# Optimization experiments

Measured on AMD Instinct MI355X. Metric: run time of the kernel, lower is better.

## Reference

```python
import jax, jax.numpy as jnp
import numpy as np

B, H, S, D = 4, 8, 2048, 64  # batch, heads, seq, head_dim (feature_dim == num_features == D)


def setup_inputs() -> dict:
    key = jax.random.key(0)
    kq, kk, kv, kw = jax.random.split(key, 4)
    return {
        "q": jax.random.normal(kq, (B, H, S, D), dtype=jnp.float32),
        "k": jax.random.normal(kk, (B, H, S, D), dtype=jnp.float32),
        "v": jax.random.normal(kv, (B, H, S, D), dtype=jnp.float32),
        "random_weights": jax.random.normal(kw, (D, D), dtype=jnp.float32),  # [feature_dim, num_features]
    }


def reference(q, k, v, random_weights):
    # F.linear(x, W) == x @ W.T ; W: [feature_dim, num_features]
    qf = jax.nn.relu(jnp.einsum('bnhd,fd->bnhf', q, random_weights))
    kf = jax.nn.relu(jnp.einsum('bnad,fd->bnaf', k, random_weights))
    # full [B, N, S_q, S_kv] score matrix (as the original materializes it)
    scores = jnp.einsum('bnhd,bnad->bnha', qf, kf)
    attn_weights = jax.nn.softmax(scores, axis=-1)
    # NOTE: faithful to the original (buggy) einsum: m is contracted only in attn,
    # so attn_output[b,n,h,d] = v[b,n,h,d] * sum_m attn[b,n,h,m]
    attn_output = jnp.einsum('bnhm,bnhd->bnhd', attn_weights, v)
    return (attn_output, attn_weights)
```

## Files before the change

### kernel.cpp

```cpp
#include <hip/hip_runtime.h>
#include <cstddef>
#include <cstdint>

#define SEQ   2048
#define DIM   64
#define NHEAD 32
#define BM    128
#define BN    128
#define NT    (SEQ / BN)
#define WLD   68

typedef __attribute__((ext_vector_type(8))) short short8v;

__device__ __forceinline__ unsigned short f2bf(float x) {
    union { float f; unsigned u; } v; v.f = x;
    unsigned r = v.u + 0x7FFFu + ((v.u >> 16) & 1u);
    return (unsigned short)(r >> 16);
}
__device__ __forceinline__ float bf2f(unsigned short h) {
    union { unsigned u; float f; } v; v.u = ((unsigned)h) << 16;
    return v.f;
}

__global__ __launch_bounds__(256) void kfsplit_kernel(const float* __restrict__ kin,
                                                      const float* __restrict__ W,
                                                      unsigned short* __restrict__ khg,
                                                      unsigned short* __restrict__ klg)
{
    __shared__ __align__(16) float Ws[64 * WLD];
    const int tid  = threadIdx.x;
    const int head = blockIdx.x >> 4;
    const int r0   = (blockIdx.x & 15) * BM;

    {
        const int f = tid >> 2, cc = (tid & 3) * 16;
        const float* gw = W + f * DIM + cc;
        #pragma unroll
        for (int kk = 0; kk < 4; ++kk)
            *reinterpret_cast<float4*>(&Ws[f * WLD + cc + kk * 4]) =
                *reinterpret_cast<const float4*>(gw + kk * 4);
    }
    __syncthreads();

    const int lane = tid & 63;
    const int wid  = tid >> 6;
    const float* kb = kin + ((size_t)head * SEQ + r0) * DIM;

    float acc0[16], acc1[16];
    #pragma unroll
    for (int j = 0; j < 16; ++j) { acc0[j] = 0.f; acc1[j] = 0.f; }

    for (int d4 = 0; d4 < 16; ++d4) {
        const float4 x0 = *reinterpret_cast<const float4*>(kb + (size_t)lane * DIM + d4 * 4);
        const float4 x1 = *reinterpret_cast<const float4*>(kb + (size_t)(64 + lane) * DIM + d4 * 4);
        #pragma unroll
        for (int j = 0; j < 16; ++j) {
            const float4 w4 = *reinterpret_cast<const float4*>(&Ws[(wid * 16 + j) * WLD + d4 * 4]);
            acc0[j] = fmaf(x0.x, w4.x, fmaf(x0.y, w4.y, fmaf(x0.z, w4.z, fmaf(x0.w, w4.w, acc0[j]))));
            acc1[j] = fmaf(x1.x, w4.x, fmaf(x1.y, w4.y, fmaf(x1.z, w4.z, fmaf(x1.w, w4.w, acc1[j]))));
        }
    }

#define SPLIT_ROW(ACC, ROWOFF)                                                          \
    do {                                                                                \
        unsigned hp[8], lp[8];                                                          \
        _Pragma("unroll")                                                               \
        for (int j2 = 0; j2 < 8; ++j2) {                                                \
            const float kf0 = fmaxf(ACC[2 * j2], 0.f);                                  \
            const float kf1 = fmaxf(ACC[2 * j2 + 1], 0.f);                              \
            const unsigned short h0 = f2bf(kf0), h1 = f2bf(kf1);                        \
            const unsigned short l0 = f2bf(kf0 - bf2f(h0));                             \
            const unsigned short l1 = f2bf(kf1 - bf2f(h1));                             \
            hp[j2] = (unsigned)h0 | ((unsigned)h1 << 16);                               \
            lp[j2] = (unsigned)l0 | ((unsigned)l1 << 16);                               \
        }                                                                               \
        unsigned short* dh = khg + ((size_t)head * SEQ + r0 + (ROWOFF)) * DIM + wid * 16; \
        unsigned short* dl = klg + ((size_t)head * SEQ + r0 + (ROWOFF)) * DIM + wid * 16; \
        uint4 a, b;                                                                     \
        a.x = hp[0]; a.y = hp[1]; a.z = hp[2]; a.w = hp[3];                             \
        b.x = hp[4]; b.y = hp[5]; b.z = hp[6]; b.w = hp[7];                             \
        *reinterpret_cast<uint4*>(dh) = a; *reinterpret_cast<uint4*>(dh + 8) = b;       \
        a.x = lp[0]; a.y = lp[1]; a.z = lp[2]; a.w = lp[3];                             \
        b.x = lp[4]; b.y = lp[5]; b.z = lp[6]; b.w = lp[7];                             \
        *reinterpret_cast<uint4*>(dl) = a; *reinterpret_cast<uint4*>(dl + 8) = b;       \
    } while (0)

    SPLIT_ROW(acc0, lane);
    SPLIT_ROW(acc1, 64 + lane);
#undef SPLIT_ROW
}

__global__ __launch_bounds__(256, 2) void attn_kernel(const float* __restrict__ q,
                                                      const float* __restrict__ W,
                                                      const unsigned short* __restrict__ khg,
                                                      const unsigned short* __restrict__ klg,
                                                      float* __restrict__ out)
{
    __shared__ __align__(16) float lds[13056];
    float* Ws = lds;
    float* qf = lds + 4352;
    unsigned short* khs = reinterpret_cast<unsigned short*>(lds);
    unsigned short* kls = reinterpret_cast<unsigned short*>(lds + 4096);
    float* mbuf = lds + 8192;
    float* lbuf = lds + 8448;

    const int tid  = threadIdx.x;
    const int head = blockIdx.x >> 4;
    const int r0   = (blockIdx.x & 15) * BM;
    const int lane = tid & 63;
    const int wid  = tid >> 6;

    {
        const int f = tid >> 2, cc = (tid & 3) * 16;
        const float* gw = W + f * DIM + cc;
        #pragma unroll
        for (int kk = 0; kk < 4; ++kk)
            *reinterpret_cast<float4*>(&Ws[f * WLD + cc + kk * 4]) =
                *reinterpret_cast<const float4*>(gw + kk * 4);
    }
    __syncthreads();

    {
        const float* qb = q + ((size_t)head * SEQ + r0) * DIM;
        float a0[16], a1[16];
        #pragma unroll
        for (int j = 0; j < 16; ++j) { a0[j] = 0.f; a1[j] = 0.f; }
        for (int d4 = 0; d4 < 16; ++d4) {
            const float4 x0 = *reinterpret_cast<const float4*>(qb + (size_t)lane * DIM + d4 * 4);
            const float4 x1 = *reinterpret_cast<const float4*>(qb + (size_t)(64 + lane) * DIM + d4 * 4);
            #pragma unroll
            for (int j = 0; j < 16; ++j) {
                const float4 w4 = *reinterpret_cast<const float4*>(&Ws[(wid * 16 + j) * WLD + d4 * 4]);
                a0[j] = fmaf(x0.x, w4.x, fmaf(x0.y, w4.y, fmaf(x0.z, w4.z, fmaf(x0.w, w4.w, a0[j]))));
                a1[j] = fmaf(x1.x, w4.x, fmaf(x1.y, w4.y, fmaf(x1.z, w4.z, fmaf(x1.w, w4.w, a1[j]))));
            }
        }
        #pragma unroll
        for (int j = 0; j < 16; ++j) {
            qf[(size_t)lane * WLD + wid * 16 + j]        = fmaxf(a0[j], 0.f);
            qf[(size_t)(64 + lane) * WLD + wid * 16 + j] = fmaxf(a1[j], 0.f);
        }
    }
    __syncthreads();

    const int lr = lane & 15, lh = lane >> 4;
    const int wrow = (wid >> 1) * 64, wcol = (wid & 1) * 64;
    short8v qh[4][2], ql[4][2];
    #pragma unroll
    for (int rf = 0; rf < 4; ++rf)
        #pragma unroll
        for (int ks = 0; ks < 2; ++ks) {
            const float* src = &qf[(size_t)(wrow + rf * 16 + lr) * WLD + ks * 32 + lh * 8];
            short8v h, l;
            #pragma unroll
            for (int e = 0; e < 8; ++e) {
                const float x = src[e];
                const unsigned short hh = f2bf(x);
                h[e] = (short)hh;
                l[e] = (short)f2bf(x - bf2f(hh));
            }
            qh[rf][ks] = h;
            ql[rf][ks] = l;
        }
    __syncthreads();

    const size_t khead = (size_t)head * SEQ * DIM;
    const int sc = tid >> 1, sf = tid & 1;
    const int wbase = sc * 128 + sf * 64;
    const int wsw = (sc & 7) << 4;

#define STAGE(T)                                                                          \
    do {                                                                                  \
        const unsigned short* srch = khg + khead + (size_t)((T) * BN + sc) * DIM + sf * 32; \
        const unsigned short* srcl = klg + khead + (size_t)((T) * BN + sc) * DIM + sf * 32; \
        _Pragma("unroll")                                                                 \
        for (int j = 0; j < 4; ++j) {                                                     \
            const uint4 vh = *reinterpret_cast<const uint4*>(srch + j * 8);               \
            const uint4 vl = *reinterpret_cast<const uint4*>(srcl + j * 8);               \
            *reinterpret_cast<uint4*>(reinterpret_cast<char*>(khs) + ((wbase + j * 16) ^ wsw)) = vh; \
            *reinterpret_cast<uint4*>(reinterpret_cast<char*>(kls) + ((wbase + j * 16) ^ wsw)) = vl; \
        }                                                                                 \
    } while (0)

#define COMPUTE_ACC()                                                                     \
    do {                                                                                  \
        _Pragma("unroll")                                                                 \
        for (int cf = 0; cf < 4; ++cf) {                                                  \
            const int c  = wcol + cf * 16 + lr;                                           \
            const int rb = c * 128 + lh * 16;                                             \
            const int sw = (c & 7) << 4;                                                  \
            const short8v bh0 = *reinterpret_cast<const short8v*>(reinterpret_cast<const char*>(khs) + ((rb) ^ sw));        \
            const short8v bh1 = *reinterpret_cast<const short8v*>(reinterpret_cast<const char*>(khs) + ((rb + 64) ^ sw));   \
            const short8v bl0 = *reinterpret_cast<const short8v*>(reinterpret_cast<const char*>(kls) + ((rb) ^ sw));        \
            const short8v bl1 = *reinterpret_cast<const short8v*>(reinterpret_cast<const char*>(kls) + ((rb + 64) ^ sw));   \
            _Pragma("unroll")                                                             \
            for (int rf = 0; rf < 4; ++rf) {                                              \
                float4 a = acc[rf][cf];                                                   \
                a = __builtin_amdgcn_mfma_f32_16x16x32_bf16(qh[rf][0], bh0, a, 0, 0, 0);  \
                a = __builtin_amdgcn_mfma_f32_16x16x32_bf16(ql[rf][0], bh0, a, 0, 0, 0);  \
                a = __builtin_amdgcn_mfma_f32_16x16x32_bf16(qh[rf][0], bl0, a, 0, 0, 0);  \
                a = __builtin_amdgcn_mfma_f32_16x16x32_bf16(qh[rf][1], bh1, a, 0, 0, 0);  \
                a = __builtin_amdgcn_mfma_f32_16x16x32_bf16(ql[rf][1], bh1, a, 0, 0, 0);  \
                a = __builtin_amdgcn_mfma_f32_16x16x32_bf16(qh[rf][1], bl1, a, 0, 0, 0);  \
                acc[rf][cf] = a;                                                          \
            }                                                                             \
        }                                                                                 \
    } while (0)

    typedef __attribute__((ext_vector_type(4))) float float4;
    float mrow[16], lrow[16];
    #pragma unroll
    for (int i = 0; i < 16; ++i) { mrow[i] = -INFINITY; lrow[i] = 0.f; }

    for (int t = 0; t < NT; ++t) {
        STAGE(t);
        __syncthreads();
        float4 acc[4][4] = {};
        COMPUTE_ACC();
        #pragma unroll
        for (int rf = 0; rf < 4; ++rf)
            #pragma unroll
            for (int q4 = 0; q4 < 4; ++q4) {
                const int i = rf * 4 + q4;
                const float v0 = acc[rf][0][q4], v1 = acc[rf][1][q4];
                const float v2 = acc[rf][2][q4], v3 = acc[rf][3][q4];
                const float tm = fmaxf(fmaxf(v0, v1), fmaxf(v2, v3));
                const float mn = fmaxf(mrow[i], tm);
                const float p = __expf(v0 - mn) + __expf(v1 - mn) +
                                __expf(v2 - mn) + __expf(v3 - mn);
                lrow[i] = lrow[i] * __expf(mrow[i] - mn) + p;
                mrow[i] = mn;
            }
        __syncthreads();
    }

    #pragma unroll
    for (int s = 0; s < 4; ++s) {
        const int msk = 1 << s;
        #pragma unroll
        for (int i = 0; i < 16; ++i) {
            const float m2 = __shfl_xor(mrow[i], msk);
            const float l2 = __shfl_xor(lrow[i], msk);
            const float mn = fmaxf(mrow[i], m2);
            lrow[i] = lrow[i] * __expf(mrow[i] - mn) + l2 * __expf(m2 - mn);
            mrow[i] = mn;
        }
    }

    if (lr == 0) {
        #pragma unroll
        for (int i = 0; i < 16; ++i) {
            const int row16 = (i >> 2) * 16 + lh * 4 + (i & 3);
            mbuf[wid * 64 + row16] = mrow[i];
            lbuf[wid * 64 + row16] = lrow[i];
        }
    }
    __syncthreads();
    {
        const int pw = wid ^ 1;
        #pragma unroll
        for (int i = 0; i < 16; ++i) {
            const int row16 = (i >> 2) * 16 + lh * 4 + (i & 3);
            const float m2 = mbuf[pw * 64 + row16];
            const float l2 = lbuf[pw * 64 + row16];
            const float mn = fmaxf(mrow[i], m2);
            lrow[i] = lrow[i] * __expf(mrow[i] - mn) + l2 * __expf(m2 - mn);
            mrow[i] = mn;
        }
    }
    #pragma unroll
    for (int i = 0; i < 16; ++i) lrow[i] = 1.0f / lrow[i];

    float* outp = out + ((size_t)head * SEQ + r0) * SEQ;
    for (int t = 0; t < NT; ++t) {
        STAGE(t);
        __syncthreads();
        float4 acc[4][4] = {};
        COMPUTE_ACC();
        const int col0 = t * BN + wcol;
        #pragma unroll
        for (int rf = 0; rf < 4; ++rf)
            #pragma unroll
            for (int q4 = 0; q4 < 4; ++q4) {
                const int i = rf * 4 + q4;
                const int row = wrow + rf * 16 + lh * 4 + q4;
                float* rp = outp + (size_t)row * SEQ + col0 + lr;
                rp[0]  = __expf(acc[rf][0][q4] - mrow[i]) * lrow[i];
                rp[16] = __expf(acc[rf][1][q4] - mrow[i]) * lrow[i];
                rp[32] = __expf(acc[rf][2][q4] - mrow[i]) * lrow[i];
                rp[48] = __expf(acc[rf][3][q4] - mrow[i]) * lrow[i];
            }
        __syncthreads();
    }
#undef STAGE
#undef COMPUTE_ACC
}

extern "C" void kernel_launch(void* const* d_in, const int* in_sizes, int n_in,
                              void* d_out, int out_size, void* d_ws, size_t ws_size,
                              hipStream_t stream)
{
    const float* q = (const float*)d_in[0];
    const float* k = (const float*)d_in[1];
    const float* v = (const float*)d_in[2];
    const float* W = (const float*)d_in[3];
    float* out = (float*)d_out;

    const size_t nkf = (size_t)NHEAD * SEQ * DIM;
    unsigned short* kh;
    if (d_ws != nullptr && ws_size >= nkf * 4u) {
        kh = (unsigned short*)d_ws;
    } else {
        kh = (unsigned short*)out;
    }
    unsigned short* kl = kh + nkf;
    float* attn = out + nkf;

    kfsplit_kernel<<<NHEAD * (SEQ / BM), 256, 0, stream>>>(k, W, kh, kl);
    attn_kernel<<<NHEAD * (SEQ / BM), 256, 0, stream>>>(q, W, kh, kl, attn);

    hipMemcpyAsync((void*)out, (const void*)v, nkf * sizeof(float),
                   hipMemcpyDeviceToDevice, stream);
}
```

Before: 675.2 us.

## Double-buffer K tiles using direct global-to-LDS async loads

Replaces the register-staged copy of the bf16 hi/lo K tiles with `global_load_lds` direct-to-LDS transfers. The XOR swizzle is now applied on the global source address, so the layout in LDS stays the same. LDS grows to two 32 KB tile buffers so the next tile's load is issued before the current tile's MFMA work, removing one barrier per iteration and hiding load latency. In exchange the block uses about 66 KB of LDS, which may limit occupancy. Correctness relies on the barrier draining the outstanding async loads before the buffer is read.

```diff
diff --git a/kernel.cpp b/kernel.cpp
--- a/kernel.cpp
+++ b/kernel.cpp
@@ -11,6 +11,7 @@
 #define WLD   68
 
 typedef __attribute__((ext_vector_type(8))) short short8v;
+typedef __attribute__((ext_vector_type(4))) float f32x4;
 
 __device__ __forceinline__ unsigned short f2bf(float x) {
     union { float f; unsigned u; } v; v.f = x;
@@ -20,6 +21,13 @@
 __device__ __forceinline__ float bf2f(unsigned short h) {
     union { unsigned u; float f; } v; v.u = ((unsigned)h) << 16;
     return v.f;
+}
+
+__device__ __forceinline__ void gl_lds16(const void* g, void* l) {
+    __builtin_amdgcn_global_load_lds(
+        (const __attribute__((address_space(1))) unsigned int*)g,
+        (__attribute__((address_space(3))) unsigned int*)l,
+        16, 0, 0);
 }
 
 __global__ __launch_bounds__(256) void kfsplit_kernel(const float* __restrict__ kin,
@@ -96,19 +104,37 @@
                                                       const unsigned short* __restrict__ klg,
                                                       float* __restrict__ out)
 {
-    __shared__ __align__(16) float lds[13056];
-    float* Ws = lds;
-    float* qf = lds + 4352;
-    unsigned short* khs = reinterpret_cast<unsigned short*>(lds);
-    unsigned short* kls = reinterpret_cast<unsigned short*>(lds + 4096);
-    float* mbuf = lds + 8192;
-    float* lbuf = lds + 8448;
+    __shared__ __align__(16) unsigned char lds_raw[67584];
+    float* Ws   = (float*)lds_raw;
+    float* qf   = (float*)(lds_raw + 32768);
+    float* mbuf = (float*)(lds_raw + 65536);
+    float* lbuf = (float*)(lds_raw + 66560);
 
     const int tid  = threadIdx.x;
     const int head = blockIdx.x >> 4;
     const int r0   = (blockIdx.x & 15) * BM;
     const int lane = tid & 63;
     const int wid  = tid >> 6;
+
+    const size_t khead_b = (size_t)head * SEQ * DIM * 2;
+    const unsigned char* gkh = (const unsigned char*)khg + khead_b;
+    const unsigned char* gkl = (const unsigned char*)klg + khead_b;
+
+#define STAGE(BUF, T)                                                                   \
+    do {                                                                                \
+        const unsigned char* skh = gkh + (size_t)(T) * (BN * DIM * 2);                  \
+        const unsigned char* skl = gkl + (size_t)(T) * (BN * DIM * 2);                  \
+        unsigned char* lkh = lds_raw + (BUF) * 32768;                                   \
+        unsigned char* lkl = lkh + 16384;                                               \
+        _Pragma("unroll")                                                               \
+        for (int i_ = 0; i_ < 4; ++i_) {                                                \
+            const unsigned o_   = wid * 4096 + i_ * 1024 + lane * 16;                   \
+            const unsigned row_ = o_ >> 7;                                              \
+            const unsigned u_   = (o_ & ~127u) | ((o_ & 127u) ^ ((row_ & 7u) << 4));    \
+            gl_lds16(skh + u_, lkh + wid * 4096 + i_ * 1024);                           \
+            gl_lds16(skl + u_, lkl + wid * 4096 + i_ * 1024);                           \
+        }                                                                               \
+    } while (0)
 
     {
         const int f = tid >> 2, cc = (tid & 3) * 16;
@@ -142,6 +168,8 @@
         }
     }
     __syncthreads();
+
+    STAGE(0, 0);
 
     const int lr = lane & 15, lh = lane >> 4;
     const int wrow = (wid >> 1) * 64, wcol = (wid & 1) * 64;
@@ -164,38 +192,22 @@
         }
     __syncthreads();
 
-    const size_t khead = (size_t)head * SEQ * DIM;
-    const int sc = tid >> 1, sf = tid & 1;
-    const int wbase = sc * 128 + sf * 64;
-    const int wsw = (sc & 7) << 4;
-
-#define STAGE(T)                                                                          \
+#define COMPUTE_ACC(BUF)                                                                  \
     do {                                                                                  \
-        const unsigned short* srch = khg + khead + (size_t)((T) * BN + sc) * DIM + sf * 32; \
-        const unsigned short* srcl = klg + khead + (size_t)((T) * BN + sc) * DIM + sf * 32; \
-        _Pragma("unroll")                                                                 \
-        for (int j = 0; j < 4; ++j) {                                                     \
-            const uint4 vh = *reinterpret_cast<const uint4*>(srch + j * 8);               \
-            const uint4 vl = *reinterpret_cast<const uint4*>(srcl + j * 8);               \
-            *reinterpret_cast<uint4*>(reinterpret_cast<char*>(khs) + ((wbase + j * 16) ^ wsw)) = vh; \
-            *reinterpret_cast<uint4*>(reinterpret_cast<char*>(kls) + ((wbase + j * 16) ^ wsw)) = vl; \
-        }                                                                                 \
-    } while (0)
-
-#define COMPUTE_ACC()                                                                     \
-    do {                                                                                  \
+        const unsigned char* khb = lds_raw + (BUF) * 32768;                               \
+        const unsigned char* klb = khb + 16384;                                           \
         _Pragma("unroll")                                                                 \
         for (int cf = 0; cf < 4; ++cf) {                                                  \
             const int c  = wcol + cf * 16 + lr;                                           \
             const int rb = c * 128 + lh * 16;                                             \
             const int sw = (c & 7) << 4;                                                  \
-            const short8v bh0 = *reinterpret_cast<const short8v*>(reinterpret_cast<const char*>(khs) + ((rb) ^ sw));        \
-            const short8v bh1 = *reinterpret_cast<const short8v*>(reinterpret_cast<const char*>(khs) + ((rb + 64) ^ sw));   \
-            const short8v bl0 = *reinterpret_cast<const short8v*>(reinterpret_cast<const char*>(kls) + ((rb) ^ sw));        \
-            const short8v bl1 = *reinterpret_cast<const short8v*>(reinterpret_cast<const char*>(kls) + ((rb + 64) ^ sw));   \
+            const short8v bh0 = *reinterpret_cast<const short8v*>(khb + ((rb) ^ sw));     \
+            const short8v bh1 = *reinterpret_cast<const short8v*>(khb + ((rb + 64) ^ sw));\
+            const short8v bl0 = *reinterpret_cast<const short8v*>(klb + ((rb) ^ sw));     \
+            const short8v bl1 = *reinterpret_cast<const short8v*>(klb + ((rb + 64) ^ sw));\
             _Pragma("unroll")                                                             \
             for (int rf = 0; rf < 4; ++rf) {                                              \
-                float4 a = acc[rf][cf];                                                   \
+                f32x4 a = acc[rf][cf];                                                    \
                 a = __builtin_amdgcn_mfma_f32_16x16x32_bf16(qh[rf][0], bh0, a, 0, 0, 0);  \
                 a = __builtin_amdgcn_mfma_f32_16x16x32_bf16(ql[rf][0], bh0, a, 0, 0, 0);  \
                 a = __builtin_amdgcn_mfma_f32_16x16x32_bf16(qh[rf][0], bl0, a, 0, 0, 0);  \
@@ -207,32 +219,36 @@
         }                                                                                 \
     } while (0)
 
-    typedef __attribute__((ext_vector_type(4))) float float4;
     float mrow[16], lrow[16];
     #pragma unroll
     for (int i = 0; i < 16; ++i) { mrow[i] = -INFINITY; lrow[i] = 0.f; }
 
-    for (int t = 0; t < NT; ++t) {
-        STAGE(t);
-        __syncthreads();
-        float4 acc[4][4] = {};
-        COMPUTE_ACC();
-        #pragma unroll
-        for (int rf = 0; rf < 4; ++rf)
+    {
+        int cur = 0;
+        for (int t = 0; t < NT; ++t) {
+            if (t + 1 < NT) STAGE(cur ^ 1, t + 1);
+            f32x4 acc[4][4] = {};
+            COMPUTE_ACC(cur);
             #pragma unroll
-            for (int q4 = 0; q4 < 4; ++q4) {
-                const int i = rf * 4 + q4;
-                const float v0 = acc[rf][0][q4], v1 = acc[rf][1][q4];
-                const float v2 = acc[rf][2][q4], v3 = acc[rf][3][q4];
-                const float tm = fmaxf(fmaxf(v0, v1), fmaxf(v2, v3));
-                const float mn = fmaxf(mrow[i], tm);
-                const float p = __expf(v0 - mn) + __expf(v1 - mn) +
-                                __expf(v2 - mn) + __expf(v3 - mn);
-                lrow[i] = lrow[i] * __expf(mrow[i] - mn) + p;
-                mrow[i] = mn;
-            }
-        __syncthreads();
-    }
+            for (int rf = 0; rf < 4; ++rf)
+                #pragma unroll
+                for (int q4 = 0; q4 < 4; ++q4) {
+                    const int i = rf * 4 + q4;
+                    const float v0 = acc[rf][0][q4], v1 = acc[rf][1][q4];
+                    const float v2 = acc[rf][2][q4], v3 = acc[rf][3][q4];
+                    const float tm = fmaxf(fmaxf(v0, v1), fmaxf(v2, v3));
+                    const float mn = fmaxf(mrow[i], tm);
+                    const float p = __expf(v0 - mn) + __expf(v1 - mn) +
+                                    __expf(v2 - mn) + __expf(v3 - mn);
+                    lrow[i] = lrow[i] * __expf(mrow[i] - mn) + p;
+                    mrow[i] = mn;
+                }
+            __syncthreads();
+            cur ^= 1;
+        }
+    }
+
+    STAGE(0, 0);
 
     #pragma unroll
     for (int s = 0; s < 4; ++s) {
@@ -272,25 +288,28 @@
     for (int i = 0; i < 16; ++i) lrow[i] = 1.0f / lrow[i];
 
     float* outp = out + ((size_t)head * SEQ + r0) * SEQ;
-    for (int t = 0; t < NT; ++t) {
-        STAGE(t);
-        __syncthreads();
-        float4 acc[4][4] = {};
-        COMPUTE_ACC();
-        const int col0 = t * BN + wcol;
-        #pragma unroll
-        for (int rf = 0; rf < 4; ++rf)
+    {
+        int cur = 0;
+        for (int t = 0; t < NT; ++t) {
+            if (t + 1 < NT) STAGE(cur ^ 1, t + 1);
+            f32x4 acc[4][4] = {};
+            COMPUTE_ACC(cur);
+            const int col0 = t * BN + wcol;
             #pragma unroll
-            for (int q4 = 0; q4 < 4; ++q4) {
-                const int i = rf * 4 + q4;
-                const int row = wrow + rf * 16 + lh * 4 + q4;
-                float* rp = outp + (size_t)row * SEQ + col0 + lr;
-                rp[0]  = __expf(acc[rf][0][q4] - mrow[i]) * lrow[i];
-                rp[16] = __expf(acc[rf][1][q4] - mrow[i]) * lrow[i];
-                rp[32] = __expf(acc[rf][2][q4] - mrow[i]) * lrow[i];
-                rp[48] = __expf(acc[rf][3][q4] - mrow[i]) * lrow[i];
-            }
-        __syncthreads();
+            for (int rf = 0; rf < 4; ++rf)
+                #pragma unroll
+                for (int q4 = 0; q4 < 4; ++q4) {
+                    const int i = rf * 4 + q4;
+                    const int row = wrow + rf * 16 + lh * 4 + q4;
+                    float* rp = outp + (size_t)row * SEQ + col0 + lr;
+                    rp[0]  = __expf(acc[rf][0][q4] - mrow[i]) * lrow[i];
+                    rp[16] = __expf(acc[rf][1][q4] - mrow[i]) * lrow[i];
+                    rp[32] = __expf(acc[rf][2][q4] - mrow[i]) * lrow[i];
+                    rp[48] = __expf(acc[rf][3][q4] - mrow[i]) * lrow[i];
+                }
+            __syncthreads();
+            cur ^= 1;
+        }
     }
 #undef STAGE
 #undef COMPUTE_ACC
```

New measurement: 653.3 us. 3.2% less time.

## Compute full score rows into LDS and do exact softmax in one pass

Applied to the files above, without the earlier changes.

Replaces the two-pass online-softmax attention kernel, which recomputed QK^T twice, with a kernel that gives each block 16 query rows. It computes the full 16x2048 score strip once with MFMA, keeps it in LDS, then does an exact max, sum and normalize before writing. K fragments now come straight from global memory into registers with double buffering, and the log2e factor is folded into qf so exp2 can be used. The price is about 131 KB of LDS per block (occupancy of one block) and K being reread by 128 blocks per head instead of 16.

```diff
diff --git a/kernel.cpp b/kernel.cpp
--- a/kernel.cpp
+++ b/kernel.cpp
@@ -2,15 +2,17 @@
 #include <cstddef>
 #include <cstdint>
 
-#define SEQ   2048
-#define DIM   64
-#define NHEAD 32
-#define BM    128
-#define BN    128
-#define NT    (SEQ / BN)
-#define WLD   68
+#define SEQ    2048
+#define DIM    64
+#define NHEAD  32
+#define BM     128
+#define STRIDE 2052
+#define LOG2E  1.44269504088896340736f
 
 typedef __attribute__((ext_vector_type(8))) short short8v;
+typedef __attribute__((ext_vector_type(4))) float f32x4;
+
+__device__ __forceinline__ float fexp2(float x) { return __builtin_amdgcn_exp2f(x); }
 
 __device__ __forceinline__ unsigned short f2bf(float x) {
     union { float f; unsigned u; } v; v.f = x;
@@ -27,7 +29,7 @@
                                                       unsigned short* __restrict__ khg,
                                                       unsigned short* __restrict__ klg)
 {
-    __shared__ __align__(16) float Ws[64 * WLD];
+    __shared__ __align__(16) float Ws[64 * 68];
     const int tid  = threadIdx.x;
     const int head = blockIdx.x >> 4;
     const int r0   = (blockIdx.x & 15) * BM;
@@ -37,7 +39,7 @@
         const float* gw = W + f * DIM + cc;
         #pragma unroll
         for (int kk = 0; kk < 4; ++kk)
-            *reinterpret_cast<float4*>(&Ws[f * WLD + cc + kk * 4]) =
+            *reinterpret_cast<float4*>(&Ws[f * 68 + cc + kk * 4]) =
                 *reinterpret_cast<const float4*>(gw + kk * 4);
     }
     __syncthreads();
@@ -55,7 +57,7 @@
         const float4 x1 = *reinterpret_cast<const float4*>(kb + (size_t)(64 + lane) * DIM + d4 * 4);
         #pragma unroll
         for (int j = 0; j < 16; ++j) {
-            const float4 w4 = *reinterpret_cast<const float4*>(&Ws[(wid * 16 + j) * WLD + d4 * 4]);
+            const float4 w4 = *reinterpret_cast<const float4*>(&Ws[(wid * 16 + j) * 68 + d4 * 4]);
             acc0[j] = fmaf(x0.x, w4.x, fmaf(x0.y, w4.y, fmaf(x0.z, w4.z, fmaf(x0.w, w4.w, acc0[j]))));
             acc1[j] = fmaf(x1.x, w4.x, fmaf(x1.y, w4.y, fmaf(x1.z, w4.z, fmaf(x1.w, w4.w, acc1[j]))));
         }
@@ -90,210 +92,143 @@
 #undef SPLIT_ROW
 }
 
-__global__ __launch_bounds__(256, 2) void attn_kernel(const float* __restrict__ q,
+__global__ __launch_bounds__(256, 1) void attn_kernel(const float* __restrict__ q,
                                                       const float* __restrict__ W,
                                                       const unsigned short* __restrict__ khg,
                                                       const unsigned short* __restrict__ klg,
                                                       float* __restrict__ out)
 {
-    __shared__ __align__(16) float lds[13056];
-    float* Ws = lds;
-    float* qf = lds + 4352;
-    unsigned short* khs = reinterpret_cast<unsigned short*>(lds);
-    unsigned short* kls = reinterpret_cast<unsigned short*>(lds + 4096);
-    float* mbuf = lds + 8192;
-    float* lbuf = lds + 8448;
+    __shared__ __align__(16) unsigned char lds_raw[16 * STRIDE * 4];
+    float* strip = (float*)lds_raw;
+    float* Ws    = (float*)lds_raw;
+    float* qf    = (float*)(lds_raw + 32768);
 
     const int tid  = threadIdx.x;
-    const int head = blockIdx.x >> 4;
-    const int r0   = (blockIdx.x & 15) * BM;
+    const int head = blockIdx.x >> 7;
+    const int r0   = (blockIdx.x & 127) * 16;
     const int lane = tid & 63;
     const int wid  = tid >> 6;
+    const int lr   = lane & 15, lh = lane >> 4;
 
     {
         const int f = tid >> 2, cc = (tid & 3) * 16;
         const float* gw = W + f * DIM + cc;
         #pragma unroll
         for (int kk = 0; kk < 4; ++kk)
-            *reinterpret_cast<float4*>(&Ws[f * WLD + cc + kk * 4]) =
+            *reinterpret_cast<float4*>(&Ws[f * 68 + cc + kk * 4]) =
                 *reinterpret_cast<const float4*>(gw + kk * 4);
     }
     __syncthreads();
 
     {
-        const float* qb = q + ((size_t)head * SEQ + r0) * DIM;
-        float a0[16], a1[16];
-        #pragma unroll
-        for (int j = 0; j < 16; ++j) { a0[j] = 0.f; a1[j] = 0.f; }
+        const int row = tid & 15;
+        const int fb  = (tid >> 4) * 4;
+        const float* qrow = q + ((size_t)head * SEQ + r0 + row) * DIM;
+        float a[4] = {0.f, 0.f, 0.f, 0.f};
         for (int d4 = 0; d4 < 16; ++d4) {
-            const float4 x0 = *reinterpret_cast<const float4*>(qb + (size_t)lane * DIM + d4 * 4);
-            const float4 x1 = *reinterpret_cast<const float4*>(qb + (size_t)(64 + lane) * DIM + d4 * 4);
+            const float4 x = *reinterpret_cast<const float4*>(qrow + d4 * 4);
+            const float xs[4] = {x.x, x.y, x.z, x.w};
             #pragma unroll
-            for (int j = 0; j < 16; ++j) {
-                const float4 w4 = *reinterpret_cast<const float4*>(&Ws[(wid * 16 + j) * WLD + d4 * 4]);
-                a0[j] = fmaf(x0.x, w4.x, fmaf(x0.y, w4.y, fmaf(x0.z, w4.z, fmaf(x0.w, w4.w, a0[j]))));
-                a1[j] = fmaf(x1.x, w4.x, fmaf(x1.y, w4.y, fmaf(x1.z, w4.z, fmaf(x1.w, w4.w, a1[j]))));
-            }
-        }
-        #pragma unroll
-        for (int j = 0; j < 16; ++j) {
-            qf[(size_t)lane * WLD + wid * 16 + j]        = fmaxf(a0[j], 0.f);
-            qf[(size_t)(64 + lane) * WLD + wid * 16 + j] = fmaxf(a1[j], 0.f);
-        }
-    }
-    __syncthreads();
-
-    const int lr = lane & 15, lh = lane >> 4;
-    const int wrow = (wid >> 1) * 64, wcol = (wid & 1) * 64;
-    short8v qh[4][2], ql[4][2];
-    #pragma unroll
-    for (int rf = 0; rf < 4; ++rf)
-        #pragma unroll
-        for (int ks = 0; ks < 2; ++ks) {
-            const float* src = &qf[(size_t)(wrow + rf * 16 + lr) * WLD + ks * 32 + lh * 8];
-            short8v h, l;
-            #pragma unroll
-            for (int e = 0; e < 8; ++e) {
-                const float x = src[e];
-                const unsigned short hh = f2bf(x);
-                h[e] = (short)hh;
-                l[e] = (short)f2bf(x - bf2f(hh));
-            }
-            qh[rf][ks] = h;
-            ql[rf][ks] = l;
-        }
-    __syncthreads();
-
-    const size_t khead = (size_t)head * SEQ * DIM;
-    const int sc = tid >> 1, sf = tid & 1;
-    const int wbase = sc * 128 + sf * 64;
-    const int wsw = (sc & 7) << 4;
-
-#define STAGE(T)                                                                          \
-    do {                                                                                  \
-        const unsigned short* srch = khg + khead + (size_t)((T) * BN + sc) * DIM + sf * 32; \
-        const unsigned short* srcl = klg + khead + (size_t)((T) * BN + sc) * DIM + sf * 32; \
-        _Pragma("unroll")                                                                 \
-        for (int j = 0; j < 4; ++j) {                                                     \
-            const uint4 vh = *reinterpret_cast<const uint4*>(srch + j * 8);               \
-            const uint4 vl = *reinterpret_cast<const uint4*>(srcl + j * 8);               \
-            *reinterpret_cast<uint4*>(reinterpret_cast<char*>(khs) + ((wbase + j * 16) ^ wsw)) = vh; \
-            *reinterpret_cast<uint4*>(reinterpret_cast<char*>(kls) + ((wbase + j * 16) ^ wsw)) = vl; \
-        }                                                                                 \
+            for (int j = 0; j < 4; ++j)
+                #pragma unroll
+                for (int u = 0; u < 4; ++u)
+                    a[j] = fmaf(xs[u], Ws[(fb + j) * 68 + d4 * 4 + u], a[j]);
+        }
+        #pragma unroll
+        for (int j = 0; j < 4; ++j)
+            qf[row * 68 + fb + j] = fmaxf(a[j] * LOG2E, 0.f);
+    }
+    __syncthreads();
+
+    short8v qh[2], ql[2];
+    #pragma unroll
+    for (int ks = 0; ks < 2; ++ks) {
+        const float* src = &qf[lr * 68 + ks * 32 + lh * 8];
+        short8v h, l;
+        #pragma unroll
+        for (int e = 0; e < 8; ++e) {
+            const float x = src[e];
+            const unsigned short hh = f2bf(x);
+            h[e] = (short)hh;
+            l[e] = (short)f2bf(x - bf2f(hh));
+        }
+        qh[ks] = h;
+        ql[ks] = l;
+    }
+    __syncthreads();
+
+    const unsigned short* khh = khg + (size_t)head * SEQ * DIM;
+    const unsigned short* khl = klg + (size_t)head * SEQ * DIM;
+    const int cb0 = wid * 512;
+
+    short8v ah[2][4][2], al[2][4][2];
+#define LOADB(BUF, B)                                                              \
+    do {                                                                           \
+        const int colb_ = cb0 + (B) * 64;                                          \
+        _Pragma("unroll")                                                          \
+        for (int cf = 0; cf < 4; ++cf) {                                           \
+            const size_t ro_ = (size_t)(colb_ + cf * 16 + lr) * DIM + lh * 8;      \
+            _Pragma("unroll")                                                      \
+            for (int ks = 0; ks < 2; ++ks) {                                       \
+                ah[BUF][cf][ks] = *reinterpret_cast<const short8v*>(khh + ro_ + ks * 32); \
+                al[BUF][cf][ks] = *reinterpret_cast<const short8v*>(khl + ro_ + ks * 32); \
+            }                                                                      \
+        }                                                                          \
     } while (0)
 
-#define COMPUTE_ACC()                                                                     \
-    do {                                                                                  \
-        _Pragma("unroll")                                                                 \
-        for (int cf = 0; cf < 4; ++cf) {                                                  \
-            const int c  = wcol + cf * 16 + lr;                                           \
-            const int rb = c * 128 + lh * 16;                                             \
-            const int sw = (c & 7) << 4;                                                  \
-            const short8v bh0 = *reinterpret_cast<const short8v*>(reinterpret_cast<const char*>(khs) + ((rb) ^ sw));        \
-            const short8v bh1 = *reinterpret_cast<const short8v*>(reinterpret_cast<const char*>(khs) + ((rb + 64) ^ sw));   \
-            const short8v bl0 = *reinterpret_cast<const short8v*>(reinterpret_cast<const char*>(kls) + ((rb) ^ sw));        \
-            const short8v bl1 = *reinterpret_cast<const short8v*>(reinterpret_cast<const char*>(kls) + ((rb + 64) ^ sw));   \
-            _Pragma("unroll")                                                             \
-            for (int rf = 0; rf < 4; ++rf) {                                              \
-                float4 a = acc[rf][cf];                                                   \
-                a = __builtin_amdgcn_mfma_f32_16x16x32_bf16(qh[rf][0], bh0, a, 0, 0, 0);  \
-                a = __builtin_amdgcn_mfma_f32_16x16x32_bf16(ql[rf][0], bh0, a, 0, 0, 0);  \
-                a = __builtin_amdgcn_mfma_f32_16x16x32_bf16(qh[rf][0], bl0, a, 0, 0, 0);  \
-                a = __builtin_amdgcn_mfma_f32_16x16x32_bf16(qh[rf][1], bh1, a, 0, 0, 0);  \
-                a = __builtin_amdgcn_mfma_f32_16x16x32_bf16(ql[rf][1], bh1, a, 0, 0, 0);  \
-                a = __builtin_amdgcn_mfma_f32_16x16x32_bf16(qh[rf][1], bl1, a, 0, 0, 0);  \
-                acc[rf][cf] = a;                                                          \
-            }                                                                             \
-        }                                                                                 \
-    } while (0)
-
-    typedef __attribute__((ext_vector_type(4))) float float4;
-    float mrow[16], lrow[16];
-    #pragma unroll
-    for (int i = 0; i < 16; ++i) { mrow[i] = -INFINITY; lrow[i] = 0.f; }
-
-    for (int t = 0; t < NT; ++t) {
-        STAGE(t);
-        __syncthreads();
-        float4 acc[4][4] = {};
-        COMPUTE_ACC();
-        #pragma unroll
-        for (int rf = 0; rf < 4; ++rf)
-            #pragma unroll
-            for (int q4 = 0; q4 < 4; ++q4) {
-                const int i = rf * 4 + q4;
-                const float v0 = acc[rf][0][q4], v1 = acc[rf][1][q4];
-                const float v2 = acc[rf][2][q4], v3 = acc[rf][3][q4];
-                const float tm = fmaxf(fmaxf(v0, v1), fmaxf(v2, v3));
-                const float mn = fmaxf(mrow[i], tm);
-                const float p = __expf(v0 - mn) + __expf(v1 - mn) +
-                                __expf(v2 - mn) + __expf(v3 - mn);
-                lrow[i] = lrow[i] * __expf(mrow[i] - mn) + p;
-                mrow[i] = mn;
-            }
-        __syncthreads();
-    }
-
-    #pragma unroll
-    for (int s = 0; s < 4; ++s) {
-        const int msk = 1 << s;
-        #pragma unroll
-        for (int i = 0; i < 16; ++i) {
-            const float m2 = __shfl_xor(mrow[i], msk);
-            const float l2 = __shfl_xor(lrow[i], msk);
-            const float mn = fmaxf(mrow[i], m2);
-            lrow[i] = lrow[i] * __expf(mrow[i] - mn) + l2 * __expf(m2 - mn);
-            mrow[i] = mn;
-        }
-    }
-
-    if (lr == 0) {
-        #pragma unroll
-        for (int i = 0; i < 16; ++i) {
-            const int row16 = (i >> 2) * 16 + lh * 4 + (i & 3);
-            mbuf[wid * 64 + row16] = mrow[i];
-            lbuf[wid * 64 + row16] = lrow[i];
-        }
-    }
-    __syncthreads();
-    {
-        const int pw = wid ^ 1;
-        #pragma unroll
-        for (int i = 0; i < 16; ++i) {
-            const int row16 = (i >> 2) * 16 + lh * 4 + (i & 3);
-            const float m2 = mbuf[pw * 64 + row16];
-            const float l2 = lbuf[pw * 64 + row16];
-            const float mn = fmaxf(mrow[i], m2);
-            lrow[i] = lrow[i] * __expf(mrow[i] - mn) + l2 * __expf(m2 - mn);
-            mrow[i] = mn;
-        }
-    }
-    #pragma unroll
-    for (int i = 0; i < 16; ++i) lrow[i] = 1.0f / lrow[i];
-
-    float* outp = out + ((size_t)head * SEQ + r0) * SEQ;
-    for (int t = 0; t < NT; ++t) {
-        STAGE(t);
-        __syncthreads();
-        float4 acc[4][4] = {};
-        COMPUTE_ACC();
-        const int col0 = t * BN + wcol;
-        #pragma unroll
-        for (int rf = 0; rf < 4; ++rf)
-            #pragma unroll
-            for (int q4 = 0; q4 < 4; ++q4) {
-                const int i = rf * 4 + q4;
-                const int row = wrow + rf * 16 + lh * 4 + q4;
-                float* rp = outp + (size_t)row * SEQ + col0 + lr;
-                rp[0]  = __expf(acc[rf][0][q4] - mrow[i]) * lrow[i];
-                rp[16] = __expf(acc[rf][1][q4] - mrow[i]) * lrow[i];
-                rp[32] = __expf(acc[rf][2][q4] - mrow[i]) * lrow[i];
-                rp[48] = __expf(acc[rf][3][q4] - mrow[i]) * lrow[i];
-            }
-        __syncthreads();
-    }
-#undef STAGE
-#undef COMPUTE_ACC
+    LOADB(0, 0);
+    #pragma unroll
+    for (int b = 0; b < 8; ++b) {
+        const int cur = b & 1;
+        if (b < 7) LOADB(cur ^ 1, b + 1);
+        #pragma unroll
+        for (int cf = 0; cf < 4; ++cf) {
+            f32x4 a = {0.f, 0.f, 0.f, 0.f};
+            a = __builtin_amdgcn_mfma_f32_16x16x32_bf16(ah[cur][cf][0], qh[0], a, 0, 0, 0);
+            a = __builtin_amdgcn_mfma_f32_16x16x32_bf16(al[cur][cf][0], qh[0], a, 0, 0, 0);
+            a = __builtin_amdgcn_mfma_f32_16x16x32_bf16(ah[cur][cf][0], ql[0], a, 0, 0, 0);
+            a = __builtin_amdgcn_mfma_f32_16x16x32_bf16(ah[cur][cf][1], qh[1], a, 0, 0, 0);
+            a = __builtin_amdgcn_mfma_f32_16x16x32_bf16(al[cur][cf][1], qh[1], a, 0, 0, 0);
+            a = __builtin_amdgcn_mfma_f32_16x16x32_bf16(ah[cur][cf][1], ql[1], a, 0, 0, 0);
+            *reinterpret_cast<f32x4*>(&strip[lr * STRIDE + cb0 + b * 64 + cf * 16 + lh * 4]) = a;
+        }
+    }
+#undef LOADB
+    __syncthreads();
+
+    #pragma unroll
+    for (int rr = 0; rr < 4; ++rr) {
+        const int row = wid * 4 + rr;
+        const float* srow = strip + row * STRIDE;
+        float mx = -INFINITY;
+        #pragma unroll
+        for (int i = 0; i < 8; ++i) {
+            const float4 v = *reinterpret_cast<const float4*>(srow + i * 256 + lane * 4);
+            mx = fmaxf(mx, fmaxf(fmaxf(v.x, v.y), fmaxf(v.z, v.w)));
+        }
+        #pragma unroll
+        for (int s = 1; s < 64; s <<= 1) mx = fmaxf(mx, __shfl_xor(mx, s));
+        float sm = 0.f;
+        #pragma unroll
+        for (int i = 0; i < 8; ++i) {
+            const float4 v = *reinterpret_cast<const float4*>(srow + i * 256 + lane * 4);
+            sm += fexp2(v.x - mx) + fexp2(v.y - mx) + fexp2(v.z - mx) + fexp2(v.w - mx);
+        }
+        #pragma unroll
+        for (int s = 1; s < 64; s <<= 1) sm += __shfl_xor(sm, s);
+        const float ri = 1.0f / sm;
+        float* orow = out + ((size_t)head * SEQ + r0 + row) * SEQ;
+        #pragma unroll
+        for (int i = 0; i < 8; ++i) {
+            const float4 v = *reinterpret_cast<const float4*>(srow + i * 256 + lane * 4);
+            float4 o;
+            o.x = fexp2(v.x - mx) * ri;
+            o.y = fexp2(v.y - mx) * ri;
+            o.z = fexp2(v.z - mx) * ri;
+            o.w = fexp2(v.w - mx) * ri;
+            *reinterpret_cast<float4*>(orow + i * 256 + lane * 4) = o;
+        }
+    }
 }
 
 extern "C" void kernel_launch(void* const* d_in, const int* in_sizes, int n_in,
@@ -317,7 +252,7 @@
     float* attn = out + nkf;
 
     kfsplit_kernel<<<NHEAD * (SEQ / BM), 256, 0, stream>>>(k, W, kh, kl);
-    attn_kernel<<<NHEAD * (SEQ / BM), 256, 0, stream>>>(q, W, kh, kl, attn);
+    attn_kernel<<<NHEAD * 128, 256, 0, stream>>>(q, W, kh, kl, attn);
 
     hipMemcpyAsync((void*)out, (const void*)v, nkf * sizeof(float),
                    hipMemcpyDeviceToDevice, stream);
```

Result: slower. 976.3 us (+44.6%).
